# Kernel tuning notes

Measured on AMD Instinct MI355X. Metric: run time of the kernel, lower is better.

The kernel has to match this reference:

```python
import jax, jax.numpy as jnp
import numpy as np

B, N, C_IN, L, C_OUT = 8, 50000, 32, 9, 64
M, NNZ = 12500, 37500


def setup_inputs() -> dict:
    key = jax.random.key(0)
    k = jax.random.split(key, 7)
    x = jax.random.normal(k[0], (B, N, C_IN), dtype=jnp.float32)
    weight = jax.random.normal(k[1], (L * C_IN, C_OUT), dtype=jnp.float32) * (1.0 / np.sqrt(L * C_IN))
    bias = jax.random.normal(k[2], (C_OUT,), dtype=jnp.float32) * 0.01
    values = jax.random.uniform(k[3], (NNZ,), dtype=jnp.float32)
    spiral_indices = jax.random.randint(k[4], (N, L), 0, N, dtype=jnp.int64)
    rows = jax.random.randint(k[5], (NNZ,), 0, M, dtype=jnp.int64)
    cols = jax.random.randint(k[6], (NNZ,), 0, N, dtype=jnp.int64)
    return {"x": x, "weight": weight, "bias": bias, "values": values,
            "spiral_indices": spiral_indices, "rows": rows, "cols": cols,
            "num_out_verts": M}


def reference(x, weight, bias, values, spiral_indices, rows, cols, num_out_verts):
    b, n, c = x.shape
    # SpiralConv: gather spiral neighborhoods, flatten, linear
    g = x[:, spiral_indices]                      # [B, N, L, C]
    g = g.reshape(b, n, -1)                       # [B, N, L*C]
    out = jnp.einsum('bnk,ko->bno', g, weight) + bias
    out = jax.nn.elu(out)                         # [B, N, C_OUT]
    # Pool: sparse down_transform (gather, scale, scatter_add)
    gathered = out[:, cols] * values[None, :, None]          # [B, NNZ, C_OUT]
    pooled = jnp.zeros((b, num_out_verts, out.shape[-1]), dtype=out.dtype)
    pooled = pooled.at[:, rows].add(gathered)                # [B, M, C_OUT]
    return pooled
```

## Files before the change

kernel.cpp:

```cpp
#include <hip/hip_runtime.h>

#define BATCH   8
#define NVERT   50000
#define CIN     32
#define LSP     9
#define COUT    64
#define MVERT   12500
#define NNZ     37500

#define NFRAG   2304
#define OUTDW   (BATCH * MVERT * COUT)

#define TILE_T  128
#define TPB     293

#define PRE_BLOCKS  6250
#define PACK_BLOCKS 9
#define ZERO_BLOCKS 6250
#define HZ_BLOCKS   49

typedef __attribute__((ext_vector_type(8))) short  short8;
typedef __attribute__((ext_vector_type(4))) float  floatx4;

static __device__ __forceinline__ unsigned short f2bf(float f) {
    union { float f; unsigned int u; } c; c.f = f;
    unsigned int u = c.u;
    return (unsigned short)((u + 0x7fffu + ((u >> 16) & 1u)) >> 16);
}

__global__ __launch_bounds__(256)
void prep_kernel(const float* __restrict__ x, const float* __restrict__ w,
                 unsigned short* __restrict__ x16, unsigned short* __restrict__ wp,
                 float* __restrict__ out, int* __restrict__ hist)
{
    const int blk = blockIdx.x;
    const int tid = threadIdx.x;
    if (blk < PRE_BLOCKS) {
        const size_t base = ((size_t)blk * 256 + tid) * 8;
        const float4* s = (const float4*)(x + base);
        float4 a = s[0], c = s[1];
        unsigned short t[8];
        t[0]=f2bf(a.x); t[1]=f2bf(a.y); t[2]=f2bf(a.z); t[3]=f2bf(a.w);
        t[4]=f2bf(c.x); t[5]=f2bf(c.y); t[6]=f2bf(c.z); t[7]=f2bf(c.w);
        *(uint4*)(x16 + base) = *(uint4*)t;
    } else if (blk < PRE_BLOCKS + PACK_BLOCKS) {
        const int f = (blk - PRE_BLOCKS) * 256 + tid;
        if (f < NFRAG) {
            int s = f >> 8, g = (f >> 6) & 3, lane = f & 63;
            int k0 = s * 32 + (lane >> 4) * 8, col = g * 16 + (lane & 15);
            unsigned short t[8];
            #pragma unroll
            for (int j = 0; j < 8; ++j)
                t[j] = f2bf(w[(size_t)(k0 + j) * COUT + col]);
            ((uint4*)wp)[f] = *(uint4*)t;
        }
    } else if (blk < PRE_BLOCKS + PACK_BLOCKS + ZERO_BLOCKS) {
        const size_t base = ((size_t)(blk - PRE_BLOCKS - PACK_BLOCKS) * 256 + tid) * 4;
        if (base < OUTDW) *(uint4*)(out + base) = (uint4){0, 0, 0, 0};
    } else {
        const int i = (blk - PRE_BLOCKS - PACK_BLOCKS - ZERO_BLOCKS) * 256 + tid;
        if (i < MVERT) hist[i] = 0;
    }
}

__global__ __launch_bounds__(256)
void hist_kernel(const int* __restrict__ rows, int* __restrict__ hist) {
    int z = blockIdx.x * 256 + threadIdx.x;
    if (z < NNZ) atomicAdd(&hist[rows[z]], 1);
}

__global__ __launch_bounds__(1024)
void scan_kernel(const int* __restrict__ hist, int* __restrict__ off2) {
    __shared__ int sh[1024];
    const int t = threadIdx.x;
    const int base = t * 13;
    int loc[13];
    int s = 0;
    #pragma unroll
    for (int j = 0; j < 13; ++j) {
        int i = base + j;
        int v = (i < MVERT) ? hist[i] : 0;
        loc[j] = s; s += v;
    }
    sh[t] = s;
    __syncthreads();
    for (int d = 1; d < 1024; d <<= 1) {
        int v = (t >= d) ? sh[t - d] : 0;
        __syncthreads();
        sh[t] += v;
        __syncthreads();
    }
    const int excl = sh[t] - s;
    #pragma unroll
    for (int j = 0; j < 13; ++j) {
        int i = base + j;
        if (i < MVERT) off2[i] = excl + loc[j];
    }
}

__global__ __launch_bounds__(256)
void scatter_kernel(const int* __restrict__ rows, const int* __restrict__ cols,
                    const float* __restrict__ vals, const int* __restrict__ spiral,
                    int* __restrict__ off2,
                    int* __restrict__ rows_s, float* __restrict__ vals_s,
                    unsigned short* __restrict__ tidx) {
    int z = blockIdx.x * 256 + threadIdx.x;
    if (z < NNZ) {
        int r = rows[z];
        int c = cols[z];
        int pos = atomicAdd(&off2[r], 1);
        rows_s[pos] = r;
        vals_s[pos] = vals[z];
        unsigned short t[16];
        #pragma unroll
        for (int s = 0; s < 9; ++s) t[s] = (unsigned short)spiral[c * LSP + s];
        #pragma unroll
        for (int s = 9; s < 16; ++s) t[s] = 0;
        uint4* dst = (uint4*)(tidx + (size_t)pos * 16);
        dst[0] = *(uint4*)t;
        dst[1] = *(uint4*)(t + 8);
    }
}

__global__ __launch_bounds__(256, 3)
void spiral_mfma6_kernel(const unsigned short* __restrict__ x16,
                         const unsigned short* __restrict__ wp,
                         const float* __restrict__ bias,
                         const unsigned short* __restrict__ tidx,
                         const int* __restrict__ rows_s,
                         const float* __restrict__ vals_s,
                         float* __restrict__ out)
{
    const int bid  = blockIdx.x;
    const int b    = bid & 7;
    const int tile = bid >> 3;
    const int tid  = threadIdx.x;
    const int w    = tid >> 6;
    const int lane = tid & 63;
    const int quad = lane >> 4;
    const int m16  = lane & 15;
    const int z0w  = tile * TILE_T + 32 * w;

    const int   zc   = min(z0w + (lane & 31), NNZ - 1);
    const int   rowv = rows_s[zc];
    const float valv = vals_s[zc];
    const uint4 p0 = *(const uint4*)(tidx + (size_t)zc * 16);
    const unsigned int p1 = *(const unsigned int*)(tidx + (size_t)zc * 16 + 8);
    int idx[9];
    idx[0] = p0.x & 0xffff;  idx[1] = p0.x >> 16;
    idx[2] = p0.y & 0xffff;  idx[3] = p0.y >> 16;
    idx[4] = p0.z & 0xffff;  idx[5] = p0.z >> 16;
    idx[6] = p0.w & 0xffff;  idx[7] = p0.w >> 16;
    idx[8] = p1 & 0xffff;

    const unsigned short* xb = x16 + (size_t)b * NVERT * CIN;

    short8 A[2][9];
    #pragma unroll
    for (int s = 0; s < 9; ++s) {
        #pragma unroll
        for (int mt = 0; mt < 2; ++mt) {
            int tix = __shfl(idx[s], mt * 16 + m16);
            A[mt][s] = *(const short8*)(xb + (size_t)tix * CIN + quad * 8);
        }
    }

    floatx4 acc[2][4];
    #pragma unroll
    for (int mt = 0; mt < 2; ++mt)
        #pragma unroll
        for (int g = 0; g < 4; ++g) acc[mt][g] = (floatx4){0.f, 0.f, 0.f, 0.f};

    #pragma unroll
    for (int s = 0; s < 9; ++s) {
        short8 bf[4];
        #pragma unroll
        for (int g = 0; g < 4; ++g)
            bf[g] = *(const short8*)(wp + (size_t)((s * 4 + g) * 64 + lane) * 8);
        #pragma unroll
        for (int mt = 0; mt < 2; ++mt)
            #pragma unroll
            for (int g = 0; g < 4; ++g)
                acc[mt][g] = __builtin_amdgcn_mfma_f32_16x16x32_bf16(A[mt][s], bf[g], acc[mt][g], 0, 0, 0);
    }

    float bs[4];
    #pragma unroll
    for (int g = 0; g < 4; ++g) bs[g] = bias[g * 16 + m16];
    float* outb = out + (size_t)b * MVERT * COUT;

    #pragma unroll
    for (int mt = 0; mt < 2; ++mt) {
        int   rr[4]; float vv[4]; bool val[4];
        #pragma unroll
        for (int r = 0; r < 4; ++r) {
            const int tsk = mt * 16 + quad * 4 + r;
            rr[r]  = __shfl(rowv, tsk);
            vv[r]  = __shfl(valv, tsk);
            val[r] = (z0w + tsk) < NNZ;
        }
        bool emit[4];
        #pragma unroll
        for (int r = 0; r < 4; ++r)
            emit[r] = (r == 3) || (!val[r + 1 > 3 ? 3 : r + 1]) || (rr[r + 1 > 3 ? 3 : r + 1] != rr[r]);
        #pragma unroll
        for (int g = 0; g < 4; ++g) {
            const int ch = g * 16 + m16;
            float s = 0.0f;
            #pragma unroll
            for (int r = 0; r < 4; ++r) {
                if (val[r]) {
                    float y = acc[mt][g][r] + bs[g];
                    y = (y > 0.0f) ? y : (__expf(y) - 1.0f);
                    s += y * vv[r];
                    if (emit[r]) {
                        atomicAdd(outb + (size_t)rr[r] * COUT + ch, s);
                        s = 0.0f;
                    }
                }
            }
        }
    }
}

extern "C" void kernel_launch(void* const* d_in, const int* in_sizes, int n_in,
                              void* d_out, int out_size, void* d_ws, size_t ws_size,
                              hipStream_t stream) {
    const float* x      = (const float*)d_in[0];
    const float* w      = (const float*)d_in[1];
    const float* bias   = (const float*)d_in[2];
    const float* vals   = (const float*)d_in[3];
    const int*   spiral = (const int*)d_in[4];
    const int*   rows   = (const int*)d_in[5];
    const int*   cols   = (const int*)d_in[6];
    float* out = (float*)d_out;

    char* base = (char*)d_ws;
    unsigned short* wp     = (unsigned short*)(base);
    unsigned short* x16    = (unsigned short*)(base + 36864);
    int*            hist   = (int*)(base + 25636864);
    int*            off2   = (int*)(base + 25686864);
    int*            rows_s = (int*)(base + 25736864);
    float*          vals_s = (float*)(base + 26036896);
    unsigned short* tidx   = (unsigned short*)(base + 26186912);

    const int prep_grid = PRE_BLOCKS + PACK_BLOCKS + ZERO_BLOCKS + HZ_BLOCKS;
    prep_kernel<<<prep_grid, 256, 0, stream>>>(x, w, x16, wp, out, hist);
    hist_kernel<<<147, 256, 0, stream>>>(rows, hist);
    scan_kernel<<<1, 1024, 0, stream>>>(hist, off2);
    scatter_kernel<<<147, 256, 0, stream>>>(rows, cols, vals, spiral, off2,
                                            rows_s, vals_s, tidx);
    spiral_mfma6_kernel<<<BATCH * TPB, 256, 0, stream>>>(x16, wp, bias, tidx,
                                                         rows_s, vals_s, out);
}
```

Baseline: 178.4 us.

## Reduce pooled rows in shared memory, fold histogram into prep, memset zeroing

The main kernel now accumulates per-row partial sums in an LDS buffer covering up to 96 consecutive sorted rows. It then writes interior rows with plain float4 stores and uses global atomics only for the two boundary rows. This is meant to cut global atomic traffic on the output. Separately, the histogram kernel is merged into the prep kernel, and output and hist are zeroed with hipMemsetAsync instead of extra blocks. The cost is added LDS use, which may reduce occupancy, and two extra __syncthreads per block.

```diff
diff --git a/kernel.cpp b/kernel.cpp
--- a/kernel.cpp
+++ b/kernel.cpp
@@ -14,10 +14,11 @@
 #define TILE_T  128
 #define TPB     293
 
-#define PRE_BLOCKS  6250
-#define PACK_BLOCKS 9
-#define ZERO_BLOCKS 6250
-#define HZ_BLOCKS   49
+#define PRE_BLOCKS   6250
+#define PACK_BLOCKS  9
+#define HISTA_BLOCKS 147
+
+#define ROWCAP  96
 
 typedef __attribute__((ext_vector_type(8))) short  short8;
 typedef __attribute__((ext_vector_type(4))) float  floatx4;
@@ -30,8 +31,9 @@
 
 __global__ __launch_bounds__(256)
 void prep_kernel(const float* __restrict__ x, const float* __restrict__ w,
+                 const int* __restrict__ rows,
                  unsigned short* __restrict__ x16, unsigned short* __restrict__ wp,
-                 float* __restrict__ out, int* __restrict__ hist)
+                 int* __restrict__ hist)
 {
     const int blk = blockIdx.x;
     const int tid = threadIdx.x;
@@ -54,19 +56,10 @@
                 t[j] = f2bf(w[(size_t)(k0 + j) * COUT + col]);
             ((uint4*)wp)[f] = *(uint4*)t;
         }
-    } else if (blk < PRE_BLOCKS + PACK_BLOCKS + ZERO_BLOCKS) {
-        const size_t base = ((size_t)(blk - PRE_BLOCKS - PACK_BLOCKS) * 256 + tid) * 4;
-        if (base < OUTDW) *(uint4*)(out + base) = (uint4){0, 0, 0, 0};
     } else {
-        const int i = (blk - PRE_BLOCKS - PACK_BLOCKS - ZERO_BLOCKS) * 256 + tid;
-        if (i < MVERT) hist[i] = 0;
-    }
-}
-
-__global__ __launch_bounds__(256)
-void hist_kernel(const int* __restrict__ rows, int* __restrict__ hist) {
-    int z = blockIdx.x * 256 + threadIdx.x;
-    if (z < NNZ) atomicAdd(&hist[rows[z]], 1);
+        const int z = (blk - PRE_BLOCKS - PACK_BLOCKS) * 256 + tid;
+        if (z < NNZ) atomicAdd(&hist[rows[z]], 1);
+    }
 }
 
 __global__ __launch_bounds__(1024)
@@ -123,7 +116,7 @@
 }
 
 __global__ __launch_bounds__(256, 3)
-void spiral_mfma6_kernel(const unsigned short* __restrict__ x16,
+void spiral_mfma7_kernel(const unsigned short* __restrict__ x16,
                          const unsigned short* __restrict__ wp,
                          const float* __restrict__ bias,
                          const unsigned short* __restrict__ tidx,
@@ -131,6 +124,8 @@
                          const float* __restrict__ vals_s,
                          float* __restrict__ out)
 {
+    __shared__ float redu[ROWCAP * COUT];
+
     const int bid  = blockIdx.x;
     const int b    = bid & 7;
     const int tile = bid >> 3;
@@ -140,6 +135,13 @@
     const int quad = lane >> 4;
     const int m16  = lane & 15;
     const int z0w  = tile * TILE_T + 32 * w;
+
+    const int z0        = tile * TILE_T;
+    const int zl        = min(z0 + TILE_T - 1, NNZ - 1);
+    const int first_row = rows_s[z0];
+    const int last_row  = rows_s[zl];
+    const int span      = last_row - first_row + 1;
+    const int lim       = min(span, ROWCAP);
 
     const int   zc   = min(z0w + (lane & 31), NNZ - 1);
     const int   rowv = rows_s[zc];
@@ -165,6 +167,9 @@
         }
     }
 
+    for (int i = tid; i < lim * COUT; i += 256) redu[i] = 0.0f;
+    __syncthreads();
+
     floatx4 acc[2][4];
     #pragma unroll
     for (int mt = 0; mt < 2; ++mt)
@@ -214,11 +219,33 @@
                     y = (y > 0.0f) ? y : (__expf(y) - 1.0f);
                     s += y * vv[r];
                     if (emit[r]) {
-                        atomicAdd(outb + (size_t)rr[r] * COUT + ch, s);
+                        const int local = rr[r] - first_row;
+                        if (local < ROWCAP)
+                            atomicAdd(&redu[local * COUT + ch], s);
+                        else
+                            atomicAdd(outb + (size_t)rr[r] * COUT + ch, s);
                         s = 0.0f;
                     }
                 }
             }
+        }
+    }
+
+    __syncthreads();
+
+    for (int i = tid; i < lim * (COUT / 4); i += 256) {
+        const int local = i >> 4;
+        const int c4    = (i & 15) * 4;
+        const int row   = first_row + local;
+        const float4 v  = *(const float4*)(redu + local * COUT + c4);
+        float* dst = outb + (size_t)row * COUT + c4;
+        if (row == first_row || row == last_row) {
+            atomicAdd(dst + 0, v.x);
+            atomicAdd(dst + 1, v.y);
+            atomicAdd(dst + 2, v.z);
+            atomicAdd(dst + 3, v.w);
+        } else {
+            *(float4*)dst = v;
         }
     }
 }
@@ -244,12 +271,14 @@
     float*          vals_s = (float*)(base + 26036896);
     unsigned short* tidx   = (unsigned short*)(base + 26186912);
 
-    const int prep_grid = PRE_BLOCKS + PACK_BLOCKS + ZERO_BLOCKS + HZ_BLOCKS;
-    prep_kernel<<<prep_grid, 256, 0, stream>>>(x, w, x16, wp, out, hist);
-    hist_kernel<<<147, 256, 0, stream>>>(rows, hist);
+    hipMemsetAsync(hist, 0, MVERT * sizeof(int), stream);
+    hipMemsetAsync(out, 0, (size_t)OUTDW * sizeof(float), stream);
+
+    const int prep_grid = PRE_BLOCKS + PACK_BLOCKS + HISTA_BLOCKS;
+    prep_kernel<<<prep_grid, 256, 0, stream>>>(x, w, rows, x16, wp, hist);
     scan_kernel<<<1, 1024, 0, stream>>>(hist, off2);
     scatter_kernel<<<147, 256, 0, stream>>>(rows, cols, vals, spiral, off2,
                                             rows_s, vals_s, tidx);
-    spiral_mfma6_kernel<<<BATCH * TPB, 256, 0, stream>>>(x16, wp, bias, tidx,
+    spiral_mfma7_kernel<<<BATCH * TPB, 256, 0, stream>>>(x16, wp, bias, tidx,
                                                          rows_s, vals_s, out);
 }
```

Result: slower. 205.0 us (+14.9%).

## Fuse setup kernels into one cooperative kernel with grid syncs

Applied to the files above, without the earlier changes.

Replaces the prep, histogram, scan and scatter kernels with a single cooperative kernel of 512 blocks that uses grid-stride loops and grid.sync() between phases. The single-block scan becomes a multi-block scan (49 blocks plus a serial pass over block sums), so launch gaps and the one-block bottleneck go away. In exchange it adds five grid-wide barriers, a cooperative-launch requirement, and fewer blocks for the bandwidth-bound convert and zero phases.

```diff
diff --git a/kernel.cpp b/kernel.cpp
--- a/kernel.cpp
+++ b/kernel.cpp
@@ -1,4 +1,7 @@
 #include <hip/hip_runtime.h>
+#include <hip/hip_cooperative_groups.h>
+
+namespace cg = cooperative_groups;
 
 #define BATCH   8
 #define NVERT   50000
@@ -14,10 +17,9 @@
 #define TILE_T  128
 #define TPB     293
 
-#define PRE_BLOCKS  6250
-#define PACK_BLOCKS 9
-#define ZERO_BLOCKS 6250
-#define HZ_BLOCKS   49
+#define SETUP_BLOCKS 512
+#define SETUP_THREADS (SETUP_BLOCKS * 256)
+#define SCAN_BLOCKS 49
 
 typedef __attribute__((ext_vector_type(8))) short  short8;
 typedef __attribute__((ext_vector_type(4))) float  floatx4;
@@ -28,84 +30,93 @@
     return (unsigned short)((u + 0x7fffu + ((u >> 16) & 1u)) >> 16);
 }
 
+__device__ int g_bsum[64];
+__device__ int g_bsumP[64];
+
 __global__ __launch_bounds__(256)
-void prep_kernel(const float* __restrict__ x, const float* __restrict__ w,
-                 unsigned short* __restrict__ x16, unsigned short* __restrict__ wp,
-                 float* __restrict__ out, int* __restrict__ hist)
+void setup_kernel(const float* __restrict__ x, const float* __restrict__ w,
+                  const int* __restrict__ rows, const int* __restrict__ cols,
+                  const float* __restrict__ vals, const int* __restrict__ spiral,
+                  unsigned short* __restrict__ x16, unsigned short* __restrict__ wp,
+                  float* __restrict__ out, int* __restrict__ hist,
+                  int* __restrict__ off2,
+                  int* __restrict__ rows_s, float* __restrict__ vals_s,
+                  unsigned short* __restrict__ tidx)
 {
+    cg::grid_group grid = cg::this_grid();
     const int blk = blockIdx.x;
     const int tid = threadIdx.x;
-    if (blk < PRE_BLOCKS) {
-        const size_t base = ((size_t)blk * 256 + tid) * 8;
+    const int gid = blk * 256 + tid;
+
+    for (int v = gid; v < 1600000; v += SETUP_THREADS) {
+        const size_t base = (size_t)v * 8;
         const float4* s = (const float4*)(x + base);
         float4 a = s[0], c = s[1];
         unsigned short t[8];
         t[0]=f2bf(a.x); t[1]=f2bf(a.y); t[2]=f2bf(a.z); t[3]=f2bf(a.w);
         t[4]=f2bf(c.x); t[5]=f2bf(c.y); t[6]=f2bf(c.z); t[7]=f2bf(c.w);
         *(uint4*)(x16 + base) = *(uint4*)t;
-    } else if (blk < PRE_BLOCKS + PACK_BLOCKS) {
-        const int f = (blk - PRE_BLOCKS) * 256 + tid;
-        if (f < NFRAG) {
-            int s = f >> 8, g = (f >> 6) & 3, lane = f & 63;
-            int k0 = s * 32 + (lane >> 4) * 8, col = g * 16 + (lane & 15);
-            unsigned short t[8];
-            #pragma unroll
-            for (int j = 0; j < 8; ++j)
-                t[j] = f2bf(w[(size_t)(k0 + j) * COUT + col]);
-            ((uint4*)wp)[f] = *(uint4*)t;
-        }
-    } else if (blk < PRE_BLOCKS + PACK_BLOCKS + ZERO_BLOCKS) {
-        const size_t base = ((size_t)(blk - PRE_BLOCKS - PACK_BLOCKS) * 256 + tid) * 4;
-        if (base < OUTDW) *(uint4*)(out + base) = (uint4){0, 0, 0, 0};
-    } else {
-        const int i = (blk - PRE_BLOCKS - PACK_BLOCKS - ZERO_BLOCKS) * 256 + tid;
-        if (i < MVERT) hist[i] = 0;
-    }
-}
-
-__global__ __launch_bounds__(256)
-void hist_kernel(const int* __restrict__ rows, int* __restrict__ hist) {
-    int z = blockIdx.x * 256 + threadIdx.x;
-    if (z < NNZ) atomicAdd(&hist[rows[z]], 1);
-}
-
-__global__ __launch_bounds__(1024)
-void scan_kernel(const int* __restrict__ hist, int* __restrict__ off2) {
-    __shared__ int sh[1024];
-    const int t = threadIdx.x;
-    const int base = t * 13;
-    int loc[13];
-    int s = 0;
-    #pragma unroll
-    for (int j = 0; j < 13; ++j) {
-        int i = base + j;
-        int v = (i < MVERT) ? hist[i] : 0;
-        loc[j] = s; s += v;
-    }
-    sh[t] = s;
-    __syncthreads();
-    for (int d = 1; d < 1024; d <<= 1) {
-        int v = (t >= d) ? sh[t - d] : 0;
+    }
+    for (int v = gid; v < OUTDW / 4; v += SETUP_THREADS)
+        *(uint4*)(out + (size_t)v * 4) = (uint4){0, 0, 0, 0};
+    if (gid < NFRAG) {
+        const int f = gid;
+        int s = f >> 8, g = (f >> 6) & 3, lane = f & 63;
+        int k0 = s * 32 + (lane >> 4) * 8, col = g * 16 + (lane & 15);
+        unsigned short t[8];
+        #pragma unroll
+        for (int j = 0; j < 8; ++j)
+            t[j] = f2bf(w[(size_t)(k0 + j) * COUT + col]);
+        ((uint4*)wp)[f] = *(uint4*)t;
+    }
+    if (gid < MVERT) hist[gid] = 0;
+
+    grid.sync();
+
+    if (gid < NNZ) atomicAdd(&hist[rows[gid]], 1);
+
+    grid.sync();
+
+    __shared__ int sh[256];
+    if (blk < SCAN_BLOCKS) {
+        const int i = blk * 256 + tid;
+        const int v = (i < MVERT) ? hist[i] : 0;
+        sh[tid] = v;
         __syncthreads();
-        sh[t] += v;
-        __syncthreads();
-    }
-    const int excl = sh[t] - s;
-    #pragma unroll
-    for (int j = 0; j < 13; ++j) {
-        int i = base + j;
-        if (i < MVERT) off2[i] = excl + loc[j];
-    }
-}
-
-__global__ __launch_bounds__(256)
-void scatter_kernel(const int* __restrict__ rows, const int* __restrict__ cols,
-                    const float* __restrict__ vals, const int* __restrict__ spiral,
-                    int* __restrict__ off2,
-                    int* __restrict__ rows_s, float* __restrict__ vals_s,
-                    unsigned short* __restrict__ tidx) {
-    int z = blockIdx.x * 256 + threadIdx.x;
-    if (z < NNZ) {
+        #pragma unroll
+        for (int d = 1; d < 256; d <<= 1) {
+            int u = (tid >= d) ? sh[tid - d] : 0;
+            __syncthreads();
+            sh[tid] += u;
+            __syncthreads();
+        }
+        const int incl = sh[tid];
+        if (i < MVERT) off2[i] = incl - v;
+        if (tid == 255) g_bsum[blk] = incl;
+    }
+
+    grid.sync();
+
+    if (blk == 0 && tid == 0) {
+        int run = 0;
+        for (int k = 0; k < SCAN_BLOCKS; ++k) {
+            int t = g_bsum[k];
+            g_bsumP[k] = run;
+            run += t;
+        }
+    }
+
+    grid.sync();
+
+    if (blk < SCAN_BLOCKS) {
+        const int i = blk * 256 + tid;
+        if (i < MVERT) off2[i] += g_bsumP[blk];
+    }
+
+    grid.sync();
+
+    if (gid < NNZ) {
+        const int z = gid;
         int r = rows[z];
         int c = cols[z];
         int pos = atomicAdd(&off2[r], 1);
@@ -244,12 +255,14 @@
     float*          vals_s = (float*)(base + 26036896);
     unsigned short* tidx   = (unsigned short*)(base + 26186912);
 
-    const int prep_grid = PRE_BLOCKS + PACK_BLOCKS + ZERO_BLOCKS + HZ_BLOCKS;
-    prep_kernel<<<prep_grid, 256, 0, stream>>>(x, w, x16, wp, out, hist);
-    hist_kernel<<<147, 256, 0, stream>>>(rows, hist);
-    scan_kernel<<<1, 1024, 0, stream>>>(hist, off2);
-    scatter_kernel<<<147, 256, 0, stream>>>(rows, cols, vals, spiral, off2,
-                                            rows_s, vals_s, tidx);
+    void* args[] = {
+        (void*)&x, (void*)&w, (void*)&rows, (void*)&cols, (void*)&vals,
+        (void*)&spiral, (void*)&x16, (void*)&wp, (void*)&out, (void*)&hist,
+        (void*)&off2, (void*)&rows_s, (void*)&vals_s, (void*)&tidx
+    };
+    hipLaunchCooperativeKernel((void*)setup_kernel, dim3(SETUP_BLOCKS),
+                               dim3(256), args, 0, stream);
+
     spiral_mfma6_kernel<<<BATCH * TPB, 256, 0, stream>>>(x16, wp, bias, tidx,
                                                          rows_s, vals_s, out);
 }
```

After: 491.4 us. +175.4%, slower.
